# Kernel optimization log

Hardware: AMD Instinct MI355X
Metric: run time of the kernel (lower is better)

The kernel has to match this reference:

```python
import jax, jax.numpy as jnp
import numpy as np

NUM_CAMS = 6
H_IMG, W_IMG = 256, 256
H_MAP, W_MAP = 64, 64
BS, N_JOINTS = 64, 20


def _compute_kp_coords(heatmap):
    # heatmap: [N, J, h_map, w_map], N = bs*num_cams
    N, J = heatmap.shape[:2]
    h = heatmap * 100.0
    flat = h.reshape(N, J, -1)
    flat = jax.nn.softmax(flat, axis=2)
    confidence = jnp.max(flat, axis=2) / jnp.sum(flat, axis=2)  # [N, J]
    hm = flat.reshape(N, J, H_MAP, W_MAP)
    mass_x = hm.sum(axis=2)  # [N, J, W] (sum over rows)
    mass_y = hm.sum(axis=3)  # [N, J, H] (sum over cols)
    x = (mass_x * jnp.arange(W_MAP, dtype=hm.dtype)).sum(axis=2)  # [N, J]
    y = (mass_y * jnp.arange(H_MAP, dtype=hm.dtype)).sum(axis=2)  # [N, J]
    kp_2d_heatmap = jnp.stack([x, y, confidence], axis=-1)  # [N, J, 3]
    # NOTE: original code scales x by h_img/h_map and y by w_img/w_map (kept faithful)
    kp_2d_croped = jnp.stack([x * (H_IMG / H_MAP), y * (W_IMG / W_MAP), confidence], axis=-1)
    return kp_2d_heatmap, kp_2d_croped


def _forward(heatmap, proj_matrices, confidences):
    kp_2d_heatmap, kp_2d_croped = _compute_kp_coords(heatmap)
    J = kp_2d_croped.shape[1]
    kpc = kp_2d_croped.reshape(BS, NUM_CAMS, J, 3)
    kph = kp_2d_heatmap.reshape(BS, NUM_CAMS, J, 3)
    conf = confidences.reshape(BS, NUM_CAMS, J)
    conf = conf / conf.sum(axis=1, keepdims=True) + 1e-5

    pts = kpc[..., :2]                    # [B, C, J, 2]
    row2 = proj_matrices[:, :, 2]         # [B, C, 4]
    # A[b,c,j] = P_row2 * (x,y)^T - P_rows01, weighted by confidence
    A = row2[:, :, None, None, :] * pts[..., None] - proj_matrices[:, :, None, :2, :]  # [B,C,J,2,4]
    A = A * conf[..., None, None]
    A = A.transpose(0, 2, 1, 3, 4).reshape(BS, J, 2 * NUM_CAMS, 4)  # [B, J, 2C, 4]

    # batched SVD of tiny 12x4 matrices; last right singular vector spans null space
    _, _, vh = jnp.linalg.svd(A, full_matrices=False)  # vh: [B, J, 4, 4]
    homo = -vh[..., 3, :]                               # [B, J, 4]
    kp_3d = homo[..., :3] / homo[..., 3:4]
    res_triang = jnp.abs(jnp.einsum('bjnk,bjk->bjn', A, homo)).sum(axis=-1)  # L1 residual
    return kp_3d, res_triang, kpc, kph


def setup_inputs() -> dict:
    key = jax.random.key(0)
    k1, k2, k3 = jax.random.split(key, 3)
    heatmap = jax.random.normal(k1, (BS * NUM_CAMS, N_JOINTS, H_MAP, W_MAP), dtype=jnp.float32)
    proj_matrices = jax.random.normal(k2, (BS, NUM_CAMS, 3, 4), dtype=jnp.float32)
    confidences = jax.random.uniform(k3, (BS * NUM_CAMS, N_JOINTS), dtype=jnp.float32)
    return {"heatmap": heatmap, "proj_matrices": proj_matrices, "confidences": confidences}


def reference(heatmap, proj_matrices, confidences):
    return _forward(heatmap, proj_matrices, confidences)
```

## Files before the change

kernel.cpp:

```cpp
#include <hip/hip_runtime.h>
#include <math.h>

#define NMAPS   7680
#define BSZ     64
#define NCAMS   6
#define NJ      20

#define OFF_KP3D 0
#define OFF_RES  3840
#define OFF_KPC  5120
#define OFF_KPH  28160

typedef float floatx4 __attribute__((ext_vector_type(4)));

__device__ __forceinline__ float waveMax(float v) {
#pragma unroll
    for (int off = 32; off > 0; off >>= 1)
        v = fmaxf(v, __shfl_down(v, off, 64));
    return v;
}

__device__ __forceinline__ double waveSum(double v) {
#pragma unroll
    for (int off = 32; off > 0; off >>= 1)
        v += __shfl_down(v, off, 64);
    return v;
}

__global__ __launch_bounds__(256) void kp_kernel(const float* __restrict__ hm,
                                                 float* __restrict__ out) {
    const int b = blockIdx.x;
    const int t = threadIdx.x;
    const floatx4* base = (const floatx4*)(hm + (size_t)b * 4096);

    floatx4 v[4];
#pragma unroll
    for (int i = 0; i < 4; i++) v[i] = __builtin_nontemporal_load(&base[t + 256 * i]);

    float m = v[0].x;
#pragma unroll
    for (int i = 0; i < 4; i++)
        m = fmaxf(m, fmaxf(fmaxf(v[i].x, v[i].y), fmaxf(v[i].z, v[i].w)));

    __shared__ float  smax[4];
    __shared__ double sred[3][4];
    const int wave = t >> 6, lane = t & 63;

    float wm = waveMax(m);
    if (lane == 0) smax[wave] = wm;
    __syncthreads();
    const float gmax = fmaxf(fmaxf(smax[0], smax[1]), fmaxf(smax[2], smax[3]));
    const float hmax = 100.0f * gmax;

    double se = 0.0, sx = 0.0, sy = 0.0;
#pragma unroll
    for (int i = 0; i < 4; i++) {
        const int idx0 = (t + 256 * i) * 4;
        const float vals[4] = {v[i].x, v[i].y, v[i].z, v[i].w};
#pragma unroll
        for (int k = 0; k < 4; k++) {
            const float e = expf(100.0f * vals[k] - hmax);
            const int idx = idx0 + k;
            se += (double)e;
            sx += (double)e * (double)(idx & 63);
            sy += (double)e * (double)(idx >> 6);
        }
    }
    se = waveSum(se); sx = waveSum(sx); sy = waveSum(sy);
    if (lane == 0) { sred[0][wave] = se; sred[1][wave] = sx; sred[2][wave] = sy; }
    __syncthreads();

    if (t == 0) {
        const double SE = sred[0][0] + sred[0][1] + sred[0][2] + sred[0][3];
        const double SX = sred[1][0] + sred[1][1] + sred[1][2] + sred[1][3];
        const double SY = sred[2][0] + sred[2][1] + sred[2][2] + sred[2][3];
        const float x    = (float)(SX / SE);
        const float y    = (float)(SY / SE);
        const float conf = (float)(1.0 / SE);
        const int o = b * 3;
        out[OFF_KPH + o + 0] = x;
        out[OFF_KPH + o + 1] = y;
        out[OFF_KPH + o + 2] = conf;
        out[OFF_KPC + o + 0] = 4.0f * x;
        out[OFF_KPC + o + 1] = 4.0f * y;
        out[OFF_KPC + o + 2] = conf;
    }
}

__global__ __launch_bounds__(256) void tri_kernel(const float* __restrict__ proj,
                                                  const float* __restrict__ confin,
                                                  float* __restrict__ out) {
    const int t = blockIdx.x * blockDim.x + threadIdx.x;
    if (t >= BSZ * NJ) return;
    const int bs = t / NJ, j = t % NJ;

    float cn[NCAMS];
    float csum = 0.0f;
#pragma unroll
    for (int c = 0; c < NCAMS; c++) {
        cn[c] = confin[(bs * NCAMS + c) * NJ + j];
        csum += cn[c];
    }
#pragma unroll
    for (int c = 0; c < NCAMS; c++) cn[c] = cn[c] / csum + 1e-5f;

    float A[12][4];
#pragma unroll
    for (int c = 0; c < NCAMS; c++) {
        const float* P = proj + ((size_t)bs * NCAMS + c) * 12;
        const int kidx = OFF_KPC + ((bs * NCAMS + c) * NJ + j) * 3;
        const float px = out[kidx + 0];
        const float py = out[kidx + 1];
#pragma unroll
        for (int k = 0; k < 4; k++) {
            const float r2 = P[8 + k];
            A[c * 2 + 0][k] = (r2 * px - P[k])     * cn[c];
            A[c * 2 + 1][k] = (r2 * py - P[4 + k]) * cn[c];
        }
    }

    double M[4][4], V[4][4];
    double diagmax = 0.0;
#pragma unroll
    for (int a = 0; a < 4; a++)
#pragma unroll
        for (int b2 = a; b2 < 4; b2++) {
            double s = 0.0;
#pragma unroll
            for (int n = 0; n < 12; n++) s += (double)A[n][a] * (double)A[n][b2];
            M[a][b2] = s; M[b2][a] = s;
            if (a == b2) diagmax = fmax(diagmax, fabs(s));
        }
#pragma unroll
    for (int a = 0; a < 4; a++)
#pragma unroll
        for (int b2 = 0; b2 < 4; b2++) V[a][b2] = (a == b2) ? 1.0 : 0.0;

    const double skip_tol = diagmax * 1e-18;
    for (int sweep = 0; sweep < 6; sweep++) {
#pragma unroll
        for (int p = 0; p < 3; p++)
#pragma unroll
            for (int q2 = p + 1; q2 < 4; q2++) {
                const double apq = M[p][q2];
                if (fabs(apq) <= skip_tol) continue;
                const double tau = (M[q2][q2] - M[p][p]) / (2.0 * apq);
                const double tt  = (tau >= 0.0 ? 1.0 : -1.0) /
                                   (fabs(tau) + sqrt(1.0 + tau * tau));
                const double c   = 1.0 / sqrt(1.0 + tt * tt);
                const double s   = tt * c;
#pragma unroll
                for (int k = 0; k < 4; k++) {
                    const double mkp = M[k][p], mkq = M[k][q2];
                    M[k][p]  = c * mkp - s * mkq;
                    M[k][q2] = s * mkp + c * mkq;
                }
#pragma unroll
                for (int k = 0; k < 4; k++) {
                    const double mpk = M[p][k], mqk = M[q2][k];
                    M[p][k]  = c * mpk - s * mqk;
                    M[q2][k] = s * mpk + c * mqk;
                }
#pragma unroll
                for (int k = 0; k < 4; k++) {
                    const double vkp = V[k][p], vkq = V[k][q2];
                    V[k][p]  = c * vkp - s * vkq;
                    V[k][q2] = s * vkp + c * vkq;
                }
            }
    }

    int mi = 0;
#pragma unroll
    for (int i = 1; i < 4; i++)
        if (M[i][i] < M[mi][mi]) mi = i;
    const double h0 = V[0][mi], h1 = V[1][mi], h2 = V[2][mi], h3 = V[3][mi];

    out[OFF_KP3D + t * 3 + 0] = (float)(h0 / h3);
    out[OFF_KP3D + t * 3 + 1] = (float)(h1 / h3);
    out[OFF_KP3D + t * 3 + 2] = (float)(h2 / h3);

    const float hf0 = (float)h0, hf1 = (float)h1, hf2 = (float)h2, hf3 = (float)h3;
    float res = 0.0f;
#pragma unroll
    for (int n = 0; n < 12; n++)
        res += fabsf(A[n][0] * hf0 + A[n][1] * hf1 + A[n][2] * hf2 + A[n][3] * hf3);
    out[OFF_RES + t] = res;
}

extern "C" void kernel_launch(void* const* d_in, const int* in_sizes, int n_in,
                              void* d_out, int out_size, void* d_ws, size_t ws_size,
                              hipStream_t stream) {
    const float* heatmap = (const float*)d_in[0];
    const float* proj    = (const float*)d_in[1];
    const float* confid  = (const float*)d_in[2];
    float* out = (float*)d_out;

    hipLaunchKernelGGL(kp_kernel, dim3(NMAPS), dim3(256), 0, stream, heatmap, out);
    hipLaunchKernelGGL(tri_kernel, dim3((BSZ * NJ + 255) / 256), dim3(256), 0, stream,
                       proj, confid, out);
}
```

Baseline: 194.9 us.

## Fuse triangulation into heatmap kernel via per-joint atomic ticket counters

Merges the two kernels into one. Each heatmap block increments a per-(batch, joint) ticket after writing its keypoint, and the last of the six camera blocks runs the SVD triangulation for that joint on a single thread. This removes the second kernel launch and its dependency gap, and adds a memset launch, atomics and fences. The tail triangulation work is serialised on one thread per block and may extend the critical path.

```diff
diff --git a/kernel.cpp b/kernel.cpp
--- a/kernel.cpp
+++ b/kernel.cpp
@@ -27,8 +27,110 @@
     return v;
 }
 
-__global__ __launch_bounds__(256) void kp_kernel(const float* __restrict__ hm,
-                                                 float* __restrict__ out) {
+__device__ void tri_solve(int bs, int j,
+                          const float* __restrict__ proj,
+                          const float* __restrict__ confin,
+                          float* __restrict__ out) {
+    float cn[NCAMS];
+    float csum = 0.0f;
+#pragma unroll
+    for (int c = 0; c < NCAMS; c++) {
+        cn[c] = confin[(bs * NCAMS + c) * NJ + j];
+        csum += cn[c];
+    }
+#pragma unroll
+    for (int c = 0; c < NCAMS; c++) cn[c] = cn[c] / csum + 1e-5f;
+
+    float A[12][4];
+#pragma unroll
+    for (int c = 0; c < NCAMS; c++) {
+        const float* P = proj + ((size_t)bs * NCAMS + c) * 12;
+        const int kidx = OFF_KPC + ((bs * NCAMS + c) * NJ + j) * 3;
+        const float px = atomicAdd(&out[kidx + 0], 0.0f);
+        const float py = atomicAdd(&out[kidx + 1], 0.0f);
+#pragma unroll
+        for (int k = 0; k < 4; k++) {
+            const float r2 = P[8 + k];
+            A[c * 2 + 0][k] = (r2 * px - P[k])     * cn[c];
+            A[c * 2 + 1][k] = (r2 * py - P[4 + k]) * cn[c];
+        }
+    }
+
+    double M[4][4], V[4][4];
+    double diagmax = 0.0;
+#pragma unroll
+    for (int a = 0; a < 4; a++)
+#pragma unroll
+        for (int b2 = a; b2 < 4; b2++) {
+            double s = 0.0;
+#pragma unroll
+            for (int n = 0; n < 12; n++) s += (double)A[n][a] * (double)A[n][b2];
+            M[a][b2] = s; M[b2][a] = s;
+            if (a == b2) diagmax = fmax(diagmax, fabs(s));
+        }
+#pragma unroll
+    for (int a = 0; a < 4; a++)
+#pragma unroll
+        for (int b2 = 0; b2 < 4; b2++) V[a][b2] = (a == b2) ? 1.0 : 0.0;
+
+    const double skip_tol = diagmax * 1e-18;
+    for (int sweep = 0; sweep < 6; sweep++) {
+#pragma unroll
+        for (int p = 0; p < 3; p++)
+#pragma unroll
+            for (int q2 = p + 1; q2 < 4; q2++) {
+                const double apq = M[p][q2];
+                if (fabs(apq) <= skip_tol) continue;
+                const double tau = (M[q2][q2] - M[p][p]) / (2.0 * apq);
+                const double tt  = (tau >= 0.0 ? 1.0 : -1.0) /
+                                   (fabs(tau) + sqrt(1.0 + tau * tau));
+                const double c   = 1.0 / sqrt(1.0 + tt * tt);
+                const double s   = tt * c;
+#pragma unroll
+                for (int k = 0; k < 4; k++) {
+                    const double mkp = M[k][p], mkq = M[k][q2];
+                    M[k][p]  = c * mkp - s * mkq;
+                    M[k][q2] = s * mkp + c * mkq;
+                }
+#pragma unroll
+                for (int k = 0; k < 4; k++) {
+                    const double mpk = M[p][k], mqk = M[q2][k];
+                    M[p][k]  = c * mpk - s * mqk;
+                    M[q2][k] = s * mpk + c * mqk;
+                }
+#pragma unroll
+                for (int k = 0; k < 4; k++) {
+                    const double vkp = V[k][p], vkq = V[k][q2];
+                    V[k][p]  = c * vkp - s * vkq;
+                    V[k][q2] = s * vkp + c * vkq;
+                }
+            }
+    }
+
+    int mi = 0;
+#pragma unroll
+    for (int i = 1; i < 4; i++)
+        if (M[i][i] < M[mi][mi]) mi = i;
+    const double h0 = V[0][mi], h1 = V[1][mi], h2 = V[2][mi], h3 = V[3][mi];
+
+    const int t = bs * NJ + j;
+    out[OFF_KP3D + t * 3 + 0] = (float)(h0 / h3);
+    out[OFF_KP3D + t * 3 + 1] = (float)(h1 / h3);
+    out[OFF_KP3D + t * 3 + 2] = (float)(h2 / h3);
+
+    const float hf0 = (float)h0, hf1 = (float)h1, hf2 = (float)h2, hf3 = (float)h3;
+    float res = 0.0f;
+#pragma unroll
+    for (int n = 0; n < 12; n++)
+        res += fabsf(A[n][0] * hf0 + A[n][1] * hf1 + A[n][2] * hf2 + A[n][3] * hf3);
+    out[OFF_RES + t] = res;
+}
+
+__global__ __launch_bounds__(256) void fused_kernel(const float* __restrict__ hm,
+                                                    const float* __restrict__ proj,
+                                                    const float* __restrict__ confin,
+                                                    float* __restrict__ out,
+                                                    unsigned* __restrict__ tickets) {
     const int b = blockIdx.x;
     const int t = threadIdx.x;
     const floatx4* base = (const floatx4*)(hm + (size_t)b * 4096);
@@ -81,111 +183,19 @@
         out[OFF_KPH + o + 0] = x;
         out[OFF_KPH + o + 1] = y;
         out[OFF_KPH + o + 2] = conf;
-        out[OFF_KPC + o + 0] = 4.0f * x;
-        out[OFF_KPC + o + 1] = 4.0f * y;
+        atomicExch(&out[OFF_KPC + o + 0], 4.0f * x);
+        atomicExch(&out[OFF_KPC + o + 1], 4.0f * y);
         out[OFF_KPC + o + 2] = conf;
-    }
-}
-
-__global__ __launch_bounds__(256) void tri_kernel(const float* __restrict__ proj,
-                                                  const float* __restrict__ confin,
-                                                  float* __restrict__ out) {
-    const int t = blockIdx.x * blockDim.x + threadIdx.x;
-    if (t >= BSZ * NJ) return;
-    const int bs = t / NJ, j = t % NJ;
-
-    float cn[NCAMS];
-    float csum = 0.0f;
-#pragma unroll
-    for (int c = 0; c < NCAMS; c++) {
-        cn[c] = confin[(bs * NCAMS + c) * NJ + j];
-        csum += cn[c];
-    }
-#pragma unroll
-    for (int c = 0; c < NCAMS; c++) cn[c] = cn[c] / csum + 1e-5f;
-
-    float A[12][4];
-#pragma unroll
-    for (int c = 0; c < NCAMS; c++) {
-        const float* P = proj + ((size_t)bs * NCAMS + c) * 12;
-        const int kidx = OFF_KPC + ((bs * NCAMS + c) * NJ + j) * 3;
-        const float px = out[kidx + 0];
-        const float py = out[kidx + 1];
-#pragma unroll
-        for (int k = 0; k < 4; k++) {
-            const float r2 = P[8 + k];
-            A[c * 2 + 0][k] = (r2 * px - P[k])     * cn[c];
-            A[c * 2 + 1][k] = (r2 * py - P[4 + k]) * cn[c];
-        }
-    }
-
-    double M[4][4], V[4][4];
-    double diagmax = 0.0;
-#pragma unroll
-    for (int a = 0; a < 4; a++)
-#pragma unroll
-        for (int b2 = a; b2 < 4; b2++) {
-            double s = 0.0;
-#pragma unroll
-            for (int n = 0; n < 12; n++) s += (double)A[n][a] * (double)A[n][b2];
-            M[a][b2] = s; M[b2][a] = s;
-            if (a == b2) diagmax = fmax(diagmax, fabs(s));
-        }
-#pragma unroll
-    for (int a = 0; a < 4; a++)
-#pragma unroll
-        for (int b2 = 0; b2 < 4; b2++) V[a][b2] = (a == b2) ? 1.0 : 0.0;
-
-    const double skip_tol = diagmax * 1e-18;
-    for (int sweep = 0; sweep < 6; sweep++) {
-#pragma unroll
-        for (int p = 0; p < 3; p++)
-#pragma unroll
-            for (int q2 = p + 1; q2 < 4; q2++) {
-                const double apq = M[p][q2];
-                if (fabs(apq) <= skip_tol) continue;
-                const double tau = (M[q2][q2] - M[p][p]) / (2.0 * apq);
-                const double tt  = (tau >= 0.0 ? 1.0 : -1.0) /
-                                   (fabs(tau) + sqrt(1.0 + tau * tau));
-                const double c   = 1.0 / sqrt(1.0 + tt * tt);
-                const double s   = tt * c;
-#pragma unroll
-                for (int k = 0; k < 4; k++) {
-                    const double mkp = M[k][p], mkq = M[k][q2];
-                    M[k][p]  = c * mkp - s * mkq;
-                    M[k][q2] = s * mkp + c * mkq;
-                }
-#pragma unroll
-                for (int k = 0; k < 4; k++) {
-                    const double mpk = M[p][k], mqk = M[q2][k];
-                    M[p][k]  = c * mpk - s * mqk;
-                    M[q2][k] = s * mpk + c * mqk;
-                }
-#pragma unroll
-                for (int k = 0; k < 4; k++) {
-                    const double vkp = V[k][p], vkq = V[k][q2];
-                    V[k][p]  = c * vkp - s * vkq;
-                    V[k][q2] = s * vkp + c * vkq;
-                }
-            }
-    }
-
-    int mi = 0;
-#pragma unroll
-    for (int i = 1; i < 4; i++)
-        if (M[i][i] < M[mi][mi]) mi = i;
-    const double h0 = V[0][mi], h1 = V[1][mi], h2 = V[2][mi], h3 = V[3][mi];
-
-    out[OFF_KP3D + t * 3 + 0] = (float)(h0 / h3);
-    out[OFF_KP3D + t * 3 + 1] = (float)(h1 / h3);
-    out[OFF_KP3D + t * 3 + 2] = (float)(h2 / h3);
-
-    const float hf0 = (float)h0, hf1 = (float)h1, hf2 = (float)h2, hf3 = (float)h3;
-    float res = 0.0f;
-#pragma unroll
-    for (int n = 0; n < 12; n++)
-        res += fabsf(A[n][0] * hf0 + A[n][1] * hf1 + A[n][2] * hf2 + A[n][3] * hf3);
-    out[OFF_RES + t] = res;
+
+        __threadfence();
+        const int n  = b / NJ, j = b % NJ;
+        const int bs = n / NCAMS;
+        const unsigned old = atomicAdd(&tickets[bs * NJ + j], 1u);
+        if (old == NCAMS - 1) {
+            __threadfence();
+            tri_solve(bs, j, proj, confin, out);
+        }
+    }
 }
 
 extern "C" void kernel_launch(void* const* d_in, const int* in_sizes, int n_in,
@@ -195,8 +205,10 @@
     const float* proj    = (const float*)d_in[1];
     const float* confid  = (const float*)d_in[2];
     float* out = (float*)d_out;
-
-    hipLaunchKernelGGL(kp_kernel, dim3(NMAPS), dim3(256), 0, stream, heatmap, out);
-    hipLaunchKernelGGL(tri_kernel, dim3((BSZ * NJ + 255) / 256), dim3(256), 0, stream,
-                       proj, confid, out);
-}
+    unsigned* tickets = (unsigned*)d_ws;
+
+    hipMemsetAsync(tickets, 0, BSZ * NJ * sizeof(unsigned), stream);
+
+    hipLaunchKernelGGL(fused_kernel, dim3(NMAPS), dim3(256), 0, stream,
+                       heatmap, proj, confid, out, tickets);
+}
```

After: 658.8 us. 238% more time.
